# Performance work log

Measured on AMD Instinct MI355X. Metric: run time of the kernel, lower is better.

## Reference

```python
import jax, jax.numpy as jnp
import numpy as np

N_NODES = 100000


def _gcn_layer(x, W, b, src, dst, norm_edge, self_norm):
    # GCNConv: out = D^{-1/2}(A+I)D^{-1/2} X W + b
    h = x @ W                                   # [N, out]
    msgs = h[src] * norm_edge[:, None]          # [E, out] gather + scale
    out = jax.ops.segment_sum(msgs, dst, num_segments=N_NODES)
    out = out + self_norm[:, None] * h          # self-loop contribution
    return out + b


def _norms(edge_index):
    src, dst = edge_index[0], edge_index[1]
    # degree includes the self-loop weight of 1 (PyG gcn_norm)
    deg = jax.ops.segment_sum(jnp.ones(src.shape[0], jnp.float32), dst,
                              num_segments=N_NODES) + 1.0
    deg_isqrt = jnp.where(deg > 0, jax.lax.rsqrt(deg), 0.0)
    norm_edge = deg_isqrt[src] * deg_isqrt[dst]  # per-edge norm
    self_norm = deg_isqrt * deg_isqrt            # norm for i->i self loop
    return src, dst, norm_edge, self_norm


def setup_inputs() -> dict:
    key = jax.random.key(0)
    ks = jax.random.split(key, 10)
    channels = [128, 64, 32]
    dims = list(zip(channels[:-1], channels[1:])) + \
           list(zip(channels[::-1][:-1], channels[::-1][1:]))  # enc + dec
    inp = {
        "x": jax.random.normal(ks[0], (N_NODES, 128), jnp.float32),
        "edge_index": jax.random.randint(ks[1], (2, 1600000), 0, N_NODES,
                                         dtype=jnp.int64),
    }
    for i, (din, dout) in enumerate(dims):
        scale = 1.0 / np.sqrt(din)
        inp[f"W{i+1}"] = jax.random.normal(ks[2 + 2 * i], (din, dout),
                                           jnp.float32) * scale
        inp[f"b{i+1}"] = jnp.zeros((dout,), jnp.float32)
    return inp


def reference(x, edge_index, W1, b1, W2, b2, W3, b3, W4, b4):
    src, dst, norm_edge, self_norm = _norms(edge_index)
    # Dropout is identity in eval mode; ReLU follows every GCNConv
    for W, b in ((W1, b1), (W2, b2), (W3, b3), (W4, b4)):
        x = jax.nn.relu(_gcn_layer(x, W, b, src, dst, norm_edge, self_norm))
    return x
```

## Files before the change

### kernel.cpp

```cpp
#include <hip/hip_runtime.h>
#include <hip/hip_fp16.h>


#define DEV static __device__ __forceinline__
#define ELL_CAP 48
#define BSHIFT 8
#define BRANGE 256
#define BCAP 5120
#define EPT 16
#define TILE (256 * EPT)
#define MAXNB 1024
#define SPILL_CAP 65536

typedef _Float16 f16x8 __attribute__((ext_vector_type(8)));
typedef float f32x4 __attribute__((ext_vector_type(4)));

DEV int eidx(const void* ei, long long i, int is64) {
  if (is64) return (int)((const long long*)ei)[i];
  return ((const int*)ei)[i];
}

__global__ void detect64_kernel(const int* __restrict__ w, long long nwords,
                                int* __restrict__ flag) {
  __shared__ int nz;
  if (threadIdx.x == 0) nz = 0;
  __syncthreads();
  long long samples = nwords / 2;
  if (samples > 4096) samples = 4096;
  for (long long i = threadIdx.x; i < samples; i += blockDim.x) {
    if (w[2 * i + 1] != 0) atomicOr(&nz, 1);
  }
  __syncthreads();
  if (threadIdx.x == 0) *flag = (nz == 0) ? 1 : 0;
}

__global__ void zero_ints(int* __restrict__ p, int n) {
  int i = blockIdx.x * blockDim.x + threadIdx.x;
  if (i < n) p[i] = 0;
}

__global__ __launch_bounds__(256) void bucket_scatter(
    const void* __restrict__ ei, const int* __restrict__ flagp, long long E,
    int* __restrict__ bcnt, unsigned int* __restrict__ bdata,
    int* __restrict__ spill_cnt, int2* __restrict__ spill, int nb) {
  __shared__ int lcnt[MAXNB];
  __shared__ int gbase[MAXNB];
  const int tid = threadIdx.x;
  const long long base = (long long)blockIdx.x * TILE;
  for (int i = tid; i < nb; i += 256) lcnt[i] = 0;
  __syncthreads();
  const int is64 = *flagp;
  unsigned upack[EPT];
  int ub[EPT];
#pragma unroll
  for (int i = 0; i < EPT; i++) {
    const long long e = base + i * 256 + tid;
    ub[i] = -1;
    if (e < E) {
      const int s = eidx(ei, e, is64);
      const int d = eidx(ei, E + e, is64);
      const int b = d >> BSHIFT;
      ub[i] = b;
      upack[i] = ((unsigned)s << BSHIFT) | (unsigned)(d & (BRANGE - 1));
      atomicAdd(&lcnt[b], 1);
    }
  }
  __syncthreads();
  for (int i = tid; i < nb; i += 256) {
    const int c = lcnt[i];
    gbase[i] = (c > 0) ? atomicAdd(&bcnt[i], c) : 0;
    lcnt[i] = 0;
  }
  __syncthreads();
#pragma unroll
  for (int i = 0; i < EPT; i++) {
    if (ub[i] >= 0) {
      const int b = ub[i];
      const int slot = atomicAdd(&lcnt[b], 1);
      const int pos = gbase[b] + slot;
      if (pos < BCAP) {
        bdata[(long long)b * BCAP + pos] = upack[i];
      } else {
        const int sp = atomicAdd(spill_cnt, 1);
        if (sp < SPILL_CAP)
          spill[sp] = make_int2((int)(upack[i] >> BSHIFT),
                                (b << BSHIFT) | (int)(upack[i] & (BRANGE - 1)));
      }
    }
  }
}

__global__ __launch_bounds__(256) void ell_build(
    const int* __restrict__ bcnt, const unsigned int* __restrict__ bdata,
    int* __restrict__ cursor, int* __restrict__ ell, int n) {
  const int b = blockIdx.x;
  const int lo = b << BSHIFT;
  const int npb = min(BRANGE, n - lo);
  __shared__ int scur[BRANGE];
  __shared__ int sell[BRANGE * ELL_CAP];
  for (int i = threadIdx.x; i < BRANGE; i += 256) scur[i] = 0;
  __syncthreads();
  const int cnt = min(bcnt[b], BCAP);
  const unsigned int* __restrict__ bd = bdata + (long long)b * BCAP;
  for (int i = threadIdx.x; i < cnt; i += 256) {
    const unsigned u = bd[i];
    const int ld = u & (BRANGE - 1);
    const int p = atomicAdd(&scur[ld], 1);
    if (p < ELL_CAP) sell[ld * ELL_CAP + p] = (int)(u >> BSHIFT);
  }
  __syncthreads();
  int4* __restrict__ e4 = (int4*)(ell + (long long)lo * ELL_CAP);
  const int4* __restrict__ s4 = (const int4*)sell;
  for (int i = threadIdx.x; i < npb * (ELL_CAP / 4); i += 256) e4[i] = s4[i];
  for (int i = threadIdx.x; i < npb; i += 256) cursor[lo + i] = scur[i];
}

__global__ void spill_fix(const int* __restrict__ spill_cnt,
                          const int2* __restrict__ spill,
                          int* __restrict__ cursor, int* __restrict__ ell) {
  const int m = min(*spill_cnt, SPILL_CAP);
  const int stride = gridDim.x * blockDim.x;
  for (int i = blockIdx.x * blockDim.x + threadIdx.x; i < m; i += stride) {
    const int2 e = spill[i];
    const int pos = atomicAdd(&cursor[e.y], 1);
    if (pos < ELL_CAP) ell[(long long)e.y * ELL_CAP + pos] = e.x;
  }
}

__global__ void dis_kernel(const int* __restrict__ cursor,
                           float* __restrict__ dis, int n) {
  int i = blockIdx.x * blockDim.x + threadIdx.x;
  if (i < n) dis[i] = rsqrtf((float)cursor[i] + 1.0f);
}

template <int DIN, int DOUT, int EPI, bool A16, bool OUTH>
__global__ __launch_bounds__(256) void gemm_mfma(
    const void* __restrict__ Av, const float* __restrict__ W,
    const float* __restrict__ bias, const float* __restrict__ dis,
    void* __restrict__ outv, int n) {
  constexpr int NCB = DOUT / 16;
  constexpr int NT = DIN / 32;
  constexpr int ROWS = 64;
  __shared__ _Float16 sA[ROWS][DIN + 8];
  __shared__ _Float16 sB[NT * NCB * 64 * 8];
  const int tid = threadIdx.x;
  for (int idx = tid; idx < NT * NCB * 64; idx += 256) {
    const int l = idx & 63;
    const int cb = (idx >> 6) % NCB;
    const int t = idx / (64 * NCB);
    const int c = cb * 16 + (l & 15);
    const int k0 = t * 32 + ((l >> 4) << 3);
    _Float16* dst = &sB[idx * 8];
#pragma unroll
    for (int j = 0; j < 8; j++) dst[j] = (_Float16)W[(k0 + j) * DOUT + c];
  }
  const int row0 = blockIdx.x * ROWS;
  if (A16) {
    const __half* A = (const __half*)Av;
    for (int idx = tid; idx < ROWS * DIN / 4; idx += 256) {
      const int r = idx / (DIN / 4);
      const int k = (idx % (DIN / 4)) * 4;
      const int gr = row0 + r;
      uint2 v = make_uint2(0u, 0u);
      if (gr < n) v = *(const uint2*)&A[(long long)gr * DIN + k];
      *(uint2*)&sA[r][k] = v;
    }
  } else {
    const float* A = (const float*)Av;
    for (int idx = tid; idx < ROWS * DIN / 4; idx += 256) {
      const int r = idx / (DIN / 4);
      const int k = (idx % (DIN / 4)) * 4;
      const int gr = row0 + r;
      float4 v = make_float4(0.f, 0.f, 0.f, 0.f);
      if (gr < n) v = *(const float4*)&A[(long long)gr * DIN + k];
      sA[r][k] = (_Float16)v.x;
      sA[r][k + 1] = (_Float16)v.y;
      sA[r][k + 2] = (_Float16)v.z;
      sA[r][k + 3] = (_Float16)v.w;
    }
  }
  __syncthreads();
  const int wv = tid >> 6;
  const int lane = tid & 63;
  const int lrow = lane & 15;
  const int lk = (lane >> 4) << 3;
  f32x4 acc[NCB];
#pragma unroll
  for (int cb = 0; cb < NCB; cb++) acc[cb] = (f32x4){0.f, 0.f, 0.f, 0.f};
#pragma unroll
  for (int t = 0; t < NT; t++) {
    const f16x8 a = *(const f16x8*)&sA[wv * 16 + lrow][t * 32 + lk];
#pragma unroll
    for (int cb = 0; cb < NCB; cb++) {
      const f16x8 b = *(const f16x8*)&sB[((t * NCB + cb) * 64 + lane) * 8];
      acc[cb] = __builtin_amdgcn_mfma_f32_16x16x32_f16(a, b, acc[cb], 0, 0, 0);
    }
  }
  const int crow0 = row0 + wv * 16 + ((lane >> 4) << 2);
  const int ccol = lane & 15;
#pragma unroll
  for (int cb = 0; cb < NCB; cb++) {
    const int col = cb * 16 + ccol;
#pragma unroll
    for (int i = 0; i < 4; i++) {
      const int gr = crow0 + i;
      if (gr < n) {
        float v = acc[cb][i];
        if (EPI == 0) {
          v *= dis[gr];
        } else {
          v = fmaxf(v + bias[col], 0.f);
          if (EPI == 2) v *= dis[gr];
        }
        if (OUTH)
          ((__half*)outv)[(long long)gr * DOUT + col] = __float2half(v);
        else
          ((float*)outv)[(long long)gr * DOUT + col] = v;
      }
    }
  }
}

DEV void acc8(float* a, const uint4& v) {
  union { uint4 u; __half2 h[4]; } cv;
  cv.u = v;
#pragma unroll
  for (int j = 0; j < 4; j++) {
    const float2 f = __half22float2(cv.h[j]);
    a[2 * j] += f.x;
    a[2 * j + 1] += f.y;
  }
}

template <int D, int EPI, bool OUT16>
__global__ __launch_bounds__(256) void aggregate(
    const int* __restrict__ cursor, const int* __restrict__ ell,
    const __half* __restrict__ g, const float* __restrict__ dis,
    const float* __restrict__ bias, void* __restrict__ outv, int n) {
  constexpr int TPN = D / 8;
  constexpr int NPB = 256 / TPN;
  const int node = blockIdx.x * NPB + threadIdx.x / TPN;
  const int c = (threadIdx.x & (TPN - 1)) * 8;
  if (node >= n) return;
  int deg = cursor[node];
  if (deg > ELL_CAP) deg = ELL_CAP;
  const int* __restrict__ row = ell + (long long)node * ELL_CAP;
  float a0[8], a1[8], a2[8], a3[8];
  {
    union { uint4 u; __half2 h[4]; } cv;
    cv.u = *(const uint4*)&g[(long long)node * D + c];
#pragma unroll
    for (int j = 0; j < 4; j++) {
      const float2 f = __half22float2(cv.h[j]);
      a0[2 * j] = f.x;
      a0[2 * j + 1] = f.y;
    }
#pragma unroll
    for (int j = 0; j < 8; j++) { a1[j] = 0.f; a2[j] = 0.f; a3[j] = 0.f; }
  }
  int p = 0;
  for (; p + 7 < deg; p += 8) {
    const int s0 = row[p + 0];
    const int s1 = row[p + 1];
    const int s2 = row[p + 2];
    const int s3 = row[p + 3];
    const int s4 = row[p + 4];
    const int s5 = row[p + 5];
    const int s6 = row[p + 6];
    const int s7 = row[p + 7];
    const uint4 v0 = *(const uint4*)&g[(long long)s0 * D + c];
    const uint4 v1 = *(const uint4*)&g[(long long)s1 * D + c];
    const uint4 v2 = *(const uint4*)&g[(long long)s2 * D + c];
    const uint4 v3 = *(const uint4*)&g[(long long)s3 * D + c];
    const uint4 v4 = *(const uint4*)&g[(long long)s4 * D + c];
    const uint4 v5 = *(const uint4*)&g[(long long)s5 * D + c];
    const uint4 v6 = *(const uint4*)&g[(long long)s6 * D + c];
    const uint4 v7 = *(const uint4*)&g[(long long)s7 * D + c];
    acc8(a0, v0); acc8(a1, v1); acc8(a2, v2); acc8(a3, v3);
    acc8(a0, v4); acc8(a1, v5); acc8(a2, v6); acc8(a3, v7);
  }
  for (; p < deg; ++p) {
    const uint4 v = *(const uint4*)&g[(long long)row[p] * D + c];
    acc8(a0, v);
  }
  float s[8];
#pragma unroll
  for (int j = 0; j < 8; j++) s[j] = (a0[j] + a1[j]) + (a2[j] + a3[j]);
  const float dn = dis[node];
  if (EPI == 0) {
#pragma unroll
    for (int j = 0; j < 8; j++) s[j] *= dn;
  } else {
#pragma unroll
    for (int j = 0; j < 8; j++) s[j] = fmaxf(dn * s[j] + bias[c + j], 0.f);
    if (EPI == 2) {
#pragma unroll
      for (int j = 0; j < 8; j++) s[j] *= dn;
    }
  }
  if (OUT16) {
    __half* oh = (__half*)outv;
    union { uint4 u; __half2 h[4]; } pk;
#pragma unroll
    for (int j = 0; j < 4; j++)
      pk.h[j] = __floats2half2_rn(s[2 * j], s[2 * j + 1]);
    *(uint4*)&oh[(long long)node * D + c] = pk.u;
  } else {
    float* op = (float*)outv;
    *(float4*)&op[(long long)node * D + c] = make_float4(s[0], s[1], s[2], s[3]);
    *(float4*)&op[(long long)node * D + c + 4] =
        make_float4(s[4], s[5], s[6], s[7]);
  }
}

extern "C" void kernel_launch(void* const* d_in, const int* in_sizes, int n_in,
                              void* d_out, int out_size, void* d_ws,
                              size_t ws_size, hipStream_t stream) {
  const float* x = (const float*)d_in[0];
  const void* ei = d_in[1];
  const float* W1 = (const float*)d_in[2];
  const float* b1 = (const float*)d_in[3];
  const float* W2 = (const float*)d_in[4];
  const float* b2 = (const float*)d_in[5];
  const float* W3 = (const float*)d_in[6];
  const float* b3 = (const float*)d_in[7];
  const float* W4 = (const float*)d_in[8];
  const float* b4 = (const float*)d_in[9];
  float* out = (float*)d_out;

  const long long E = (long long)in_sizes[1] / 2;
  const int N = in_sizes[0] / 128;
  const int NB = (N + BRANGE - 1) / BRANGE;
  const int NTILES = (int)((E + TILE - 1) / TILE);

  char* ws = (char*)d_ws;
  auto align256 = [](size_t o) { return (o + 255) & ~(size_t)255; };
  size_t off = 0;
  int* flag = (int*)(ws + off);      off = align256(off + 16);
  int* cursor = (int*)(ws + off);    off = align256(off + (size_t)N * 4);
  float* dis = (float*)(ws + off);   off = align256(off + (size_t)N * 4);
  int* bmeta = (int*)(ws + off);     off = align256(off + ((size_t)NB + 16) * 4);
  int2* spill = (int2*)(ws + off);   off = align256(off + (size_t)SPILL_CAP * 8);
  unsigned int* bdata = (unsigned int*)(ws + off);
  off = align256(off + (size_t)NB * BCAP * 4);
  int* ell = (int*)(ws + off);       off = align256(off + (size_t)N * ELL_CAP * 4);
  __half* gh1 = (__half*)(ws + off); off = align256(off + (size_t)N * 64 * 2);
  __half* gh2 = (__half*)(ws + off); off = align256(off + (size_t)N * 32 * 2);
  __half* gh3 = (__half*)(ws + off); off = align256(off + (size_t)N * 32 * 2);
  __half* gh4 = (__half*)(ws + off); off = align256(off + (size_t)N * 64 * 2);
  __half* oh1 = (__half*)(ws + off); off = align256(off + (size_t)N * 64 * 2);
  __half* zh3 = (__half*)(ws + off); off = align256(off + (size_t)N * 32 * 2);
  __half* zh4 = (__half*)(ws + off); off = align256(off + (size_t)N * 64 * 2);
  int* bcnt = bmeta;
  int* spill_cnt = bmeta + NB;
  (void)ws_size; (void)n_in; (void)out_size;

  const int GB = (N + 63) / 64;

  detect64_kernel<<<1, 256, 0, stream>>>((const int*)ei, 2 * E, flag);
  zero_ints<<<(NB + 16 + 255) / 256, 256, 0, stream>>>(bmeta, NB + 16);
  bucket_scatter<<<NTILES, 256, 0, stream>>>(ei, flag, E, bcnt, bdata,
                                             spill_cnt, spill, NB);
  ell_build<<<NB, 256, 0, stream>>>(bcnt, bdata, cursor, ell, N);
  spill_fix<<<64, 256, 0, stream>>>(spill_cnt, spill, cursor, ell);
  dis_kernel<<<(N + 255) / 256, 256, 0, stream>>>(cursor, dis, N);

  gemm_mfma<128, 64, 0, false, true><<<GB, 256, 0, stream>>>(
      x, W1, nullptr, dis, gh1, N);
  aggregate<64, 1, true><<<(N + 31) / 32, 256, 0, stream>>>(
      cursor, ell, gh1, dis, b1, oh1, N);
  gemm_mfma<64, 32, 0, true, true><<<GB, 256, 0, stream>>>(
      oh1, W2, nullptr, dis, gh2, N);
  aggregate<32, 2, true><<<(N + 63) / 64, 256, 0, stream>>>(
      cursor, ell, gh2, dis, b2, gh3, N);
  aggregate<32, 0, true><<<(N + 63) / 64, 256, 0, stream>>>(
      cursor, ell, gh3, dis, nullptr, zh3, N);
  gemm_mfma<32, 64, 2, true, true><<<GB, 256, 0, stream>>>(
      zh3, W3, b3, dis, gh4, N);
  aggregate<64, 0, true><<<(N + 31) / 32, 256, 0, stream>>>(
      cursor, ell, gh4, dis, nullptr, zh4, N);
  gemm_mfma<64, 128, 1, true, false><<<GB, 256, 0, stream>>>(
      zh4, W4, b4, dis, out, N);
}
```

Baseline: 239.5 us.

## Fuse graph build with first GEMM and merge small prep kernels

The first-layer GEMM no longer depends on degree normalisation, so it runs in the same launch as the edge bucket scatter: blocks are split by index between GEMM and scatter. Because of that, the first aggregation applies the source-node and destination-node normalisation itself. The zeroing of bucket metadata moves into the format-detection kernel, and the rsqrt degree computation moves into ell_build and spill_fix, removing three launches. The cost is a per-edge dis[] gather in the first aggregation. The spill path sets dis with an atomicMin, which may be fragile.

```diff
diff --git a/kernel.cpp b/kernel.cpp
--- a/kernel.cpp
+++ b/kernel.cpp
@@ -20,11 +20,13 @@
   return ((const int*)ei)[i];
 }
 
-__global__ void detect64_kernel(const int* __restrict__ w, long long nwords,
-                                int* __restrict__ flag) {
+__global__ void prep_kernel(const int* __restrict__ w, long long nwords,
+                            int* __restrict__ flag, int* __restrict__ bmeta,
+                            int nmeta) {
   __shared__ int nz;
   if (threadIdx.x == 0) nz = 0;
   __syncthreads();
+  for (int i = threadIdx.x; i < nmeta; i += blockDim.x) bmeta[i] = 0;
   long long samples = nwords / 2;
   if (samples > 4096) samples = 4096;
   for (long long i = threadIdx.x; i < samples; i += blockDim.x) {
@@ -34,19 +36,15 @@
   if (threadIdx.x == 0) *flag = (nz == 0) ? 1 : 0;
 }
 
-__global__ void zero_ints(int* __restrict__ p, int n) {
-  int i = blockIdx.x * blockDim.x + threadIdx.x;
-  if (i < n) p[i] = 0;
-}
-
-__global__ __launch_bounds__(256) void bucket_scatter(
-    const void* __restrict__ ei, const int* __restrict__ flagp, long long E,
-    int* __restrict__ bcnt, unsigned int* __restrict__ bdata,
-    int* __restrict__ spill_cnt, int2* __restrict__ spill, int nb) {
-  __shared__ int lcnt[MAXNB];
-  __shared__ int gbase[MAXNB];
+DEV void scatter_body(char* smem, const void* __restrict__ ei,
+                      const int* __restrict__ flagp, long long E,
+                      int* __restrict__ bcnt, unsigned int* __restrict__ bdata,
+                      int* __restrict__ spill_cnt, int2* __restrict__ spill,
+                      int nb, int bx) {
+  int* lcnt = (int*)smem;
+  int* gbase = lcnt + MAXNB;
   const int tid = threadIdx.x;
-  const long long base = (long long)blockIdx.x * TILE;
+  const long long base = (long long)bx * TILE;
   for (int i = tid; i < nb; i += 256) lcnt[i] = 0;
   __syncthreads();
   const int is64 = *flagp;
@@ -90,59 +88,16 @@
   }
 }
 
-__global__ __launch_bounds__(256) void ell_build(
-    const int* __restrict__ bcnt, const unsigned int* __restrict__ bdata,
-    int* __restrict__ cursor, int* __restrict__ ell, int n) {
-  const int b = blockIdx.x;
-  const int lo = b << BSHIFT;
-  const int npb = min(BRANGE, n - lo);
-  __shared__ int scur[BRANGE];
-  __shared__ int sell[BRANGE * ELL_CAP];
-  for (int i = threadIdx.x; i < BRANGE; i += 256) scur[i] = 0;
-  __syncthreads();
-  const int cnt = min(bcnt[b], BCAP);
-  const unsigned int* __restrict__ bd = bdata + (long long)b * BCAP;
-  for (int i = threadIdx.x; i < cnt; i += 256) {
-    const unsigned u = bd[i];
-    const int ld = u & (BRANGE - 1);
-    const int p = atomicAdd(&scur[ld], 1);
-    if (p < ELL_CAP) sell[ld * ELL_CAP + p] = (int)(u >> BSHIFT);
-  }
-  __syncthreads();
-  int4* __restrict__ e4 = (int4*)(ell + (long long)lo * ELL_CAP);
-  const int4* __restrict__ s4 = (const int4*)sell;
-  for (int i = threadIdx.x; i < npb * (ELL_CAP / 4); i += 256) e4[i] = s4[i];
-  for (int i = threadIdx.x; i < npb; i += 256) cursor[lo + i] = scur[i];
-}
-
-__global__ void spill_fix(const int* __restrict__ spill_cnt,
-                          const int2* __restrict__ spill,
-                          int* __restrict__ cursor, int* __restrict__ ell) {
-  const int m = min(*spill_cnt, SPILL_CAP);
-  const int stride = gridDim.x * blockDim.x;
-  for (int i = blockIdx.x * blockDim.x + threadIdx.x; i < m; i += stride) {
-    const int2 e = spill[i];
-    const int pos = atomicAdd(&cursor[e.y], 1);
-    if (pos < ELL_CAP) ell[(long long)e.y * ELL_CAP + pos] = e.x;
-  }
-}
-
-__global__ void dis_kernel(const int* __restrict__ cursor,
-                           float* __restrict__ dis, int n) {
-  int i = blockIdx.x * blockDim.x + threadIdx.x;
-  if (i < n) dis[i] = rsqrtf((float)cursor[i] + 1.0f);
-}
-
 template <int DIN, int DOUT, int EPI, bool A16, bool OUTH>
-__global__ __launch_bounds__(256) void gemm_mfma(
-    const void* __restrict__ Av, const float* __restrict__ W,
-    const float* __restrict__ bias, const float* __restrict__ dis,
-    void* __restrict__ outv, int n) {
+DEV void gemm_body(char* smem, const void* __restrict__ Av,
+                   const float* __restrict__ W, const float* __restrict__ bias,
+                   const float* __restrict__ dis, void* __restrict__ outv,
+                   int n, int bx) {
   constexpr int NCB = DOUT / 16;
   constexpr int NT = DIN / 32;
   constexpr int ROWS = 64;
-  __shared__ _Float16 sA[ROWS][DIN + 8];
-  __shared__ _Float16 sB[NT * NCB * 64 * 8];
+  _Float16(*sA)[DIN + 8] = (_Float16(*)[DIN + 8])smem;
+  _Float16* sB = (_Float16*)(smem + (size_t)ROWS * (DIN + 8) * 2);
   const int tid = threadIdx.x;
   for (int idx = tid; idx < NT * NCB * 64; idx += 256) {
     const int l = idx & 63;
@@ -154,7 +109,7 @@
 #pragma unroll
     for (int j = 0; j < 8; j++) dst[j] = (_Float16)W[(k0 + j) * DOUT + c];
   }
-  const int row0 = blockIdx.x * ROWS;
+  const int row0 = bx * ROWS;
   if (A16) {
     const __half* A = (const __half*)Av;
     for (int idx = tid; idx < ROWS * DIN / 4; idx += 256) {
@@ -208,7 +163,7 @@
         float v = acc[cb][i];
         if (EPI == 0) {
           v *= dis[gr];
-        } else {
+        } else if (EPI >= 1) {
           v = fmaxf(v + bias[col], 0.f);
           if (EPI == 2) v *= dis[gr];
         }
@@ -218,6 +173,77 @@
           ((float*)outv)[(long long)gr * DOUT + col] = v;
       }
     }
+  }
+}
+
+template <int DIN, int DOUT, int EPI, bool A16, bool OUTH>
+__global__ __launch_bounds__(256) void gemm_mfma(
+    const void* __restrict__ Av, const float* __restrict__ W,
+    const float* __restrict__ bias, const float* __restrict__ dis,
+    void* __restrict__ outv, int n) {
+  constexpr int SM = 64 * (DIN + 8) * 2 + (DIN / 32) * (DOUT / 16) * 64 * 8 * 2;
+  __shared__ __align__(16) char smem[SM];
+  gemm_body<DIN, DOUT, EPI, A16, OUTH>(smem, Av, W, bias, dis, outv, n,
+                                       blockIdx.x);
+}
+
+__global__ __launch_bounds__(256) void fused_scatter_gemm(
+    const void* __restrict__ Av, const float* __restrict__ W,
+    void* __restrict__ outv, int n, int gb,
+    const void* __restrict__ ei, const int* __restrict__ flagp, long long E,
+    int* __restrict__ bcnt, unsigned int* __restrict__ bdata,
+    int* __restrict__ spill_cnt, int2* __restrict__ spill, int nb) {
+  __shared__ __align__(16) char smem[33792];
+  if ((int)blockIdx.x < gb) {
+    gemm_body<128, 64, -1, false, true>(smem, Av, W, nullptr, nullptr, outv, n,
+                                        blockIdx.x);
+  } else {
+    scatter_body(smem, ei, flagp, E, bcnt, bdata, spill_cnt, spill, nb,
+                 blockIdx.x - gb);
+  }
+}
+
+__global__ __launch_bounds__(256) void ell_build(
+    const int* __restrict__ bcnt, const unsigned int* __restrict__ bdata,
+    int* __restrict__ cursor, int* __restrict__ ell, float* __restrict__ dis,
+    int n) {
+  const int b = blockIdx.x;
+  const int lo = b << BSHIFT;
+  const int npb = min(BRANGE, n - lo);
+  __shared__ int scur[BRANGE];
+  __shared__ int sell[BRANGE * ELL_CAP];
+  for (int i = threadIdx.x; i < BRANGE; i += 256) scur[i] = 0;
+  __syncthreads();
+  const int cnt = min(bcnt[b], BCAP);
+  const unsigned int* __restrict__ bd = bdata + (long long)b * BCAP;
+  for (int i = threadIdx.x; i < cnt; i += 256) {
+    const unsigned u = bd[i];
+    const int ld = u & (BRANGE - 1);
+    const int p = atomicAdd(&scur[ld], 1);
+    if (p < ELL_CAP) sell[ld * ELL_CAP + p] = (int)(u >> BSHIFT);
+  }
+  __syncthreads();
+  int4* __restrict__ e4 = (int4*)(ell + (long long)lo * ELL_CAP);
+  const int4* __restrict__ s4 = (const int4*)sell;
+  for (int i = threadIdx.x; i < npb * (ELL_CAP / 4); i += 256) e4[i] = s4[i];
+  for (int i = threadIdx.x; i < npb; i += 256) {
+    cursor[lo + i] = scur[i];
+    dis[lo + i] = rsqrtf((float)scur[i] + 1.0f);
+  }
+}
+
+__global__ void spill_fix(const int* __restrict__ spill_cnt,
+                          const int2* __restrict__ spill,
+                          int* __restrict__ cursor, int* __restrict__ ell,
+                          float* __restrict__ dis) {
+  const int m = min(*spill_cnt, SPILL_CAP);
+  const int stride = gridDim.x * blockDim.x;
+  for (int i = blockIdx.x * blockDim.x + threadIdx.x; i < m; i += stride) {
+    const int2 e = spill[i];
+    const int pos = atomicAdd(&cursor[e.y], 1);
+    if (pos < ELL_CAP) ell[(long long)e.y * ELL_CAP + pos] = e.x;
+    const float cand = rsqrtf((float)(pos + 1) + 1.0f);
+    atomicMin((unsigned int*)&dis[e.y], __float_as_uint(cand));
   }
 }
 
@@ -311,6 +337,76 @@
     *(float4*)&op[(long long)node * D + c + 4] =
         make_float4(s[4], s[5], s[6], s[7]);
   }
+}
+
+__global__ __launch_bounds__(256) void aggregate1_raw(
+    const int* __restrict__ cursor, const int* __restrict__ ell,
+    const __half* __restrict__ g, const float* __restrict__ dis,
+    const float* __restrict__ bias, void* __restrict__ outv, int n) {
+  constexpr int D = 64;
+  constexpr int TPN = D / 8;
+  constexpr int NPB = 256 / TPN;
+  const int node = blockIdx.x * NPB + threadIdx.x / TPN;
+  const int c = (threadIdx.x & (TPN - 1)) * 8;
+  if (node >= n) return;
+  int deg = cursor[node];
+  if (deg > ELL_CAP) deg = ELL_CAP;
+  const int* __restrict__ row = ell + (long long)node * ELL_CAP;
+  const float dn = dis[node];
+  float a0[8], a1[8];
+  {
+    union { uint4 u; __half2 h[4]; } cv;
+    cv.u = *(const uint4*)&g[(long long)node * D + c];
+#pragma unroll
+    for (int j = 0; j < 4; j++) {
+      const float2 f = __half22float2(cv.h[j]);
+      a0[2 * j] = dn * f.x;
+      a0[2 * j + 1] = dn * f.y;
+    }
+#pragma unroll
+    for (int j = 0; j < 8; j++) a1[j] = 0.f;
+  }
+  int p = 0;
+  for (; p + 1 < deg; p += 2) {
+    const int s0 = row[p];
+    const int s1 = row[p + 1];
+    const float d0 = dis[s0];
+    const float d1 = dis[s1];
+    union { uint4 u; __half2 h[4]; } c0, c1;
+    c0.u = *(const uint4*)&g[(long long)s0 * D + c];
+    c1.u = *(const uint4*)&g[(long long)s1 * D + c];
+#pragma unroll
+    for (int j = 0; j < 4; j++) {
+      const float2 f0 = __half22float2(c0.h[j]);
+      const float2 f1 = __half22float2(c1.h[j]);
+      a0[2 * j] += d0 * f0.x;
+      a0[2 * j + 1] += d0 * f0.y;
+      a1[2 * j] += d1 * f1.x;
+      a1[2 * j + 1] += d1 * f1.y;
+    }
+  }
+  for (; p < deg; ++p) {
+    const int s0 = row[p];
+    const float d0 = dis[s0];
+    union { uint4 u; __half2 h[4]; } c0;
+    c0.u = *(const uint4*)&g[(long long)s0 * D + c];
+#pragma unroll
+    for (int j = 0; j < 4; j++) {
+      const float2 f0 = __half22float2(c0.h[j]);
+      a0[2 * j] += d0 * f0.x;
+      a0[2 * j + 1] += d0 * f0.y;
+    }
+  }
+  float s[8];
+#pragma unroll
+  for (int j = 0; j < 8; j++)
+    s[j] = fmaxf(dn * (a0[j] + a1[j]) + bias[c + j], 0.f);
+  __half* oh = (__half*)outv;
+  union { uint4 u; __half2 h[4]; } pk;
+#pragma unroll
+  for (int j = 0; j < 4; j++)
+    pk.h[j] = __floats2half2_rn(s[2 * j], s[2 * j + 1]);
+  *(uint4*)&oh[(long long)node * D + c] = pk.u;
 }
 
 extern "C" void kernel_launch(void* const* d_in, const int* in_sizes, int n_in,
@@ -357,17 +453,14 @@
 
   const int GB = (N + 63) / 64;
 
-  detect64_kernel<<<1, 256, 0, stream>>>((const int*)ei, 2 * E, flag);
-  zero_ints<<<(NB + 16 + 255) / 256, 256, 0, stream>>>(bmeta, NB + 16);
-  bucket_scatter<<<NTILES, 256, 0, stream>>>(ei, flag, E, bcnt, bdata,
-                                             spill_cnt, spill, NB);
-  ell_build<<<NB, 256, 0, stream>>>(bcnt, bdata, cursor, ell, N);
-  spill_fix<<<64, 256, 0, stream>>>(spill_cnt, spill, cursor, ell);
-  dis_kernel<<<(N + 255) / 256, 256, 0, stream>>>(cursor, dis, N);
-
-  gemm_mfma<128, 64, 0, false, true><<<GB, 256, 0, stream>>>(
-      x, W1, nullptr, dis, gh1, N);
-  aggregate<64, 1, true><<<(N + 31) / 32, 256, 0, stream>>>(
+  prep_kernel<<<1, 256, 0, stream>>>((const int*)ei, 2 * E, flag, bmeta,
+                                     NB + 16);
+  fused_scatter_gemm<<<GB + NTILES, 256, 0, stream>>>(
+      x, W1, gh1, N, GB, ei, flag, E, bcnt, bdata, spill_cnt, spill, NB);
+  ell_build<<<NB, 256, 0, stream>>>(bcnt, bdata, cursor, ell, dis, N);
+  spill_fix<<<64, 256, 0, stream>>>(spill_cnt, spill, cursor, ell, dis);
+
+  aggregate1_raw<<<(N + 31) / 32, 256, 0, stream>>>(
       cursor, ell, gh1, dis, b1, oh1, N);
   gemm_mfma<64, 32, 0, true, true><<<GB, 256, 0, stream>>>(
       oh1, W2, nullptr, dis, gh2, N);
```

Result: faster. 223.0 us (-6.9%).
